# Kernel optimization log

Hardware: AMD Instinct MI355X
Metric: run time of the kernel (lower is better)

The kernel has to match this reference:

```python
import jax, jax.numpy as jnp
import numpy as np

EMB = 1024
HEADS = 16
B, N = 2, 2048

def setup_inputs() -> dict:
    key = jax.random.key(0)
    ks = jax.random.split(key, 9)
    s = 1.0 / np.sqrt(EMB)
    return {
        "x": jax.random.normal(ks[0], (B, N, EMB), dtype=jnp.float32),
        "Wq": jax.random.normal(ks[1], (EMB, EMB), dtype=jnp.float32) * s,
        "bq": jax.random.normal(ks[2], (EMB,), dtype=jnp.float32) * 0.01,
        "Wk": jax.random.normal(ks[3], (EMB, EMB), dtype=jnp.float32) * s,
        "bk": jax.random.normal(ks[4], (EMB,), dtype=jnp.float32) * 0.01,
        "Wv": jax.random.normal(ks[5], (EMB, EMB), dtype=jnp.float32) * s,
        "bv": jax.random.normal(ks[6], (EMB,), dtype=jnp.float32) * 0.01,
        "Wo": jax.random.normal(ks[7], (EMB, EMB), dtype=jnp.float32) * s,
        "bo": jax.random.normal(ks[8], (EMB,), dtype=jnp.float32) * 0.01,
    }

def _split_heads(t):
    b, n, e = t.shape
    return t.reshape(b, n, HEADS, e // HEADS).transpose(0, 2, 1, 3)  # b h n d

def reference(x, Wq, bq, Wk, bk, Wv, bv, Wo, bo):
    q = _split_heads(x @ Wq + bq)
    k = _split_heads(x @ Wk + bk)
    v = _split_heads(x @ Wv + bv)
    # NOTE: original scales by sqrt(emb_size), not sqrt(head_dim)
    scaling = jnp.asarray(EMB, x.dtype) ** 0.5
    energy = jnp.einsum('bhqd,bhkd->bhqk', q, k)
    att = jax.nn.softmax(energy / scaling, axis=-1)
    out = jnp.einsum('bhqk,bhkd->bhqd', att, v)
    out = out.transpose(0, 2, 1, 3).reshape(x.shape[0], x.shape[1], EMB)
    return out @ Wo + bo
```

## Files before the change

### kernel.cpp

```cpp
#include <hip/hip_runtime.h>
#include <hip/hip_bf16.h>

typedef __bf16 bf16_t;
typedef bf16_t bf16x4 __attribute__((ext_vector_type(4)));
typedef bf16_t bf16x8 __attribute__((ext_vector_type(8)));
typedef float f32x4 __attribute__((ext_vector_type(4)));

#define EMB 1024
#define HEADS 16
#define BATCH 2
#define SEQ 2048
#define HD 64
#define TOKENS (BATCH * SEQ)

__device__ __forceinline__ void gld16(bf16_t* lds_dst, const bf16_t* g_src) {
    __builtin_amdgcn_global_load_lds(
        (const __attribute__((address_space(1))) unsigned int*)g_src,
        (__attribute__((address_space(3))) unsigned int*)lds_dst, 16, 0, 0);
}

__global__ __launch_bounds__(256) void convert_x(const float* __restrict__ x,
                                                 bf16_t* __restrict__ xb) {
    size_t i = ((size_t)blockIdx.x * 256 + threadIdx.x) * 16;
    f32x4 v0 = *(const f32x4*)&x[i];
    f32x4 v1 = *(const f32x4*)&x[i + 4];
    f32x4 v2 = *(const f32x4*)&x[i + 8];
    f32x4 v3 = *(const f32x4*)&x[i + 12];
    bf16x8 o0, o1;
#pragma unroll
    for (int j = 0; j < 4; ++j) {
        o0[j] = (bf16_t)v0[j]; o0[4 + j] = (bf16_t)v1[j];
        o1[j] = (bf16_t)v2[j]; o1[4 + j] = (bf16_t)v3[j];
    }
    *(bf16x8*)&xb[i] = o0;
    *(bf16x8*)&xb[i + 8] = o1;
}

__global__ __launch_bounds__(256) void prep_w(
    const float* __restrict__ W0, const float* __restrict__ W1,
    const float* __restrict__ W2, const float* __restrict__ W3,
    bf16_t* __restrict__ T0, bf16_t* __restrict__ T1,
    bf16_t* __restrict__ T2, bf16_t* __restrict__ T3) {
    __shared__ __align__(16) bf16_t T[64][72];
    int z = blockIdx.z;
    const float* src = (z == 0) ? W0 : (z == 1) ? W1 : (z == 2) ? W2 : W3;
    bf16_t* dst = (z == 0) ? T0 : (z == 1) ? T1 : (z == 2) ? T2 : T3;
    int k0 = blockIdx.y * 64, n0 = blockIdx.x * 64;
    int r = threadIdx.x >> 2, c4 = (threadIdx.x & 3) * 16;
    f32x4 v[4];
#pragma unroll
    for (int q = 0; q < 4; ++q)
        v[q] = *(const f32x4*)&src[(size_t)(k0 + r) * 1024 + n0 + c4 + q * 4];
#pragma unroll
    for (int j = 0; j < 16; ++j) T[c4 + j][r] = (bf16_t)v[j >> 2][j & 3];
    __syncthreads();
    bf16x8 o0 = *(const bf16x8*)&T[r][c4];
    bf16x8 o1 = *(const bf16x8*)&T[r][c4 + 8];
    *(bf16x8*)&dst[(size_t)(n0 + r) * 1024 + k0 + c4] = o0;
    *(bf16x8*)&dst[(size_t)(n0 + r) * 1024 + k0 + c4 + 8] = o1;
}

template <typename TO>
__global__ __launch_bounds__(256) void gemm128(
    const bf16_t* __restrict__ A,
    const bf16_t* __restrict__ Wt0, const bf16_t* __restrict__ Wt1, const bf16_t* __restrict__ Wt2,
    const float* __restrict__ b0, const float* __restrict__ b1, const float* __restrict__ b2,
    TO* __restrict__ o0, TO* __restrict__ o1, TO* __restrict__ o2,
    int md0, int md1, int md2, float sc0, float sc1, float sc2) {
    __shared__ __align__(16) bf16_t As[128 * 64];
    __shared__ __align__(16) bf16_t Bs[128 * 64];

    const int tid = threadIdx.x, w = tid >> 6, lane = tid & 63;
    const int quad = lane >> 4, c = lane & 15;
    const int wm = (w >> 1) * 64, wn = (w & 1) * 64;
    const int m0 = blockIdx.y * 128, n0 = blockIdx.x * 128;

    const int z = blockIdx.z;
    const bf16_t* W = (z == 0) ? Wt0 : (z == 1) ? Wt1 : Wt2;
    const float* bias = (z == 0) ? b0 : (z == 1) ? b1 : b2;
    TO* out = (z == 0) ? o0 : (z == 1) ? o1 : o2;
    const int mode = (z == 0) ? md0 : (z == 1) ? md1 : md2;
    const float scale = (z == 0) ? sc0 : (z == 1) ? sc1 : sc2;

    f32x4 acc[4][4];
#pragma unroll
    for (int i = 0; i < 4; ++i)
#pragma unroll
        for (int j = 0; j < 4; ++j) acc[i][j] = (f32x4){0.f, 0.f, 0.f, 0.f};

    const int srow = lane >> 3, sch = lane & 7;
    const int scol = (sch ^ srow) * 8;
    const bf16_t* Ag = A + (size_t)m0 * 1024;
    const bf16_t* Bg = W + (size_t)n0 * 1024;

    for (int k0 = 0; k0 < 1024; k0 += 64) {
        __syncthreads();
#pragma unroll
        for (int s = 0; s < 4; ++s) {
            int rg = (w * 4 + s) * 8;
            gld16(&As[rg * 64], &Ag[(size_t)(rg + srow) * 1024 + k0 + scol]);
            gld16(&Bs[rg * 64], &Bg[(size_t)(rg + srow) * 1024 + k0 + scol]);
        }
        __syncthreads();

#pragma unroll
        for (int ks = 0; ks < 2; ++ks) {
            bf16x8 af[4], bfv[4];
#pragma unroll
            for (int t = 0; t < 4; ++t)
                af[t] = *(const bf16x8*)&As[(wm + t * 16 + c) * 64 +
                                            (((ks * 4 + quad) ^ (c & 7)) * 8)];
#pragma unroll
            for (int t = 0; t < 4; ++t)
                bfv[t] = *(const bf16x8*)&Bs[(wn + t * 16 + c) * 64 +
                                             (((ks * 4 + quad) ^ (c & 7)) * 8)];
#pragma unroll
            for (int mt = 0; mt < 4; ++mt)
#pragma unroll
                for (int nt = 0; nt < 4; ++nt)
                    acc[mt][nt] = __builtin_amdgcn_mfma_f32_16x16x32_bf16(
                        af[mt], bfv[nt], acc[mt][nt], 0, 0, 0);
        }
    }

#pragma unroll
    for (int nt = 0; nt < 4; ++nt) {
        int col = n0 + wn + nt * 16 + c;
        float bv = bias[col];
#pragma unroll
        for (int mt = 0; mt < 4; ++mt)
#pragma unroll
            for (int r = 0; r < 4; ++r) {
                int row = m0 + wm + mt * 16 + quad * 4 + r;
                float v = (acc[mt][nt][r] + bv) * scale;
                size_t idx;
                if (mode == 0) {
                    idx = (size_t)row * 1024 + col;
                } else {
                    int bb = row >> 11, n = row & 2047;
                    int hh = col >> 6, d = col & 63;
                    idx = (mode == 1) ? ((size_t)(bb * HEADS + hh) * SEQ + n) * HD + d
                                      : ((size_t)(bb * HEADS + hh) * HD + d) * SEQ + n;
                }
                out[idx] = (TO)v;
            }
    }
}

__global__ __launch_bounds__(256) void attn_kernel(
    const bf16_t* __restrict__ Q, const bf16_t* __restrict__ K,
    const bf16_t* __restrict__ Vt, bf16_t* __restrict__ O) {
    __shared__ __align__(16) bf16_t Ks[128 * 64];
    __shared__ __align__(16) bf16_t Vs[64 * 128];
    __shared__ __align__(16) bf16_t Ps[4][2][16][72];
    __shared__ float Lbuf[2][2][64];

    const int tid = threadIdx.x, w = tid >> 6, lane = tid & 63;
    const int quad = lane >> 4, c = lane & 15;
    const int qh = w & 1, kh = w >> 1;
    const int bh = blockIdx.x, b = bh >> 4, h = bh & 15;
    const int q0 = blockIdx.y * 64;

    const bf16_t* Qg = Q + ((size_t)bh * SEQ + q0) * HD;
    bf16x8 qf[2][2];
#pragma unroll
    for (int u = 0; u < 2; ++u)
#pragma unroll
        for (int ks = 0; ks < 2; ++ks)
            qf[u][ks] = *(const bf16x8*)&Qg[(qh * 32 + u * 16 + c) * 64 + ks * 32 + quad * 8];

    f32x4 Oacc[2][4];
#pragma unroll
    for (int u = 0; u < 2; ++u)
#pragma unroll
        for (int t = 0; t < 4; ++t) Oacc[u][t] = (f32x4){0.f, 0.f, 0.f, 0.f};
    float lp[2] = {0.f, 0.f};

    const int kr = lane >> 3, kch = lane & 7;
    const int vr = lane >> 4, vch = lane & 15;

    for (int j0 = 0; j0 < SEQ; j0 += 128) {
        __syncthreads();
        const bf16_t* Kg = K + ((size_t)bh * SEQ + j0) * HD;
        const bf16_t* Vg = Vt + (size_t)bh * HD * SEQ + j0;
#pragma unroll
        for (int s = 0; s < 4; ++s) {
            int krg = w * 32 + s * 8, krow = krg + kr;
            gld16(&Ks[krg * 64], &Kg[(size_t)krow * 64 + (kch ^ (krow & 7)) * 8]);
            int vrg = w * 16 + s * 4, vrow = vrg + vr;
            gld16(&Vs[vrg * 128], &Vg[(size_t)vrow * SEQ + (vch ^ (vrow & 15)) * 8]);
        }
        __syncthreads();

        f32x4 S[2][4];
#pragma unroll
        for (int u = 0; u < 2; ++u)
#pragma unroll
            for (int t = 0; t < 4; ++t) S[u][t] = (f32x4){0.f, 0.f, 0.f, 0.f};
#pragma unroll
        for (int ks = 0; ks < 2; ++ks)
#pragma unroll
            for (int t = 0; t < 4; ++t) {
                int row = kh * 64 + t * 16 + c;
                bf16x8 kv = *(const bf16x8*)&Ks[row * 64 + (((ks * 4 + quad) ^ (c & 7)) * 8)];
                S[0][t] = __builtin_amdgcn_mfma_f32_16x16x32_bf16(kv, qf[0][ks], S[0][t], 0, 0, 0);
                S[1][t] = __builtin_amdgcn_mfma_f32_16x16x32_bf16(kv, qf[1][ks], S[1][t], 0, 0, 0);
            }

#pragma unroll
        for (int u = 0; u < 2; ++u)
#pragma unroll
            for (int t = 0; t < 4; ++t) {
                bf16x4 pk;
#pragma unroll
                for (int r = 0; r < 4; ++r) {
                    float p = __builtin_amdgcn_exp2f(S[u][t][r]);
                    lp[u] += p;
                    pk[r] = (bf16_t)p;
                }
                *(bf16x4*)&Ps[w][u][c][t * 16 + quad * 4] = pk;
            }

#pragma unroll
        for (int ks2 = 0; ks2 < 2; ++ks2) {
            bf16x8 af0 = *(const bf16x8*)&Ps[w][0][c][ks2 * 32 + quad * 8];
            bf16x8 af1 = *(const bf16x8*)&Ps[w][1][c][ks2 * 32 + quad * 8];
#pragma unroll
            for (int t = 0; t < 4; ++t) {
                int row = t * 16 + c;
                bf16x8 vv = *(const bf16x8*)&Vs[row * 128 + (((kh * 8 + ks2 * 4 + quad) ^ c) * 8)];
                Oacc[0][t] = __builtin_amdgcn_mfma_f32_16x16x32_bf16(af0, vv, Oacc[0][t], 0, 0, 0);
                Oacc[1][t] = __builtin_amdgcn_mfma_f32_16x16x32_bf16(af1, vv, Oacc[1][t], 0, 0, 0);
            }
        }
    }

#pragma unroll
    for (int u = 0; u < 2; ++u) {
        lp[u] += __shfl_xor(lp[u], 16);
        lp[u] += __shfl_xor(lp[u], 32);
    }

    __syncthreads();
    float* Obuf = (float*)Ks;
    if (kh == 1) {
#pragma unroll
        for (int u = 0; u < 2; ++u) {
#pragma unroll
            for (int t = 0; t < 4; ++t)
                *(f32x4*)&Obuf[(((qh * 2 + u) * 4 + t) * 64 + lane) * 4] = Oacc[u][t];
            Lbuf[qh][u][lane] = lp[u];
        }
    }
    __syncthreads();
    if (kh == 0) {
        float lr[2][4];
#pragma unroll
        for (int u = 0; u < 2; ++u) {
            lp[u] += Lbuf[qh][u][lane];
#pragma unroll
            for (int r = 0; r < 4; ++r) lr[u][r] = __shfl(lp[u], quad * 4 + r);
        }
#pragma unroll
        for (int u = 0; u < 2; ++u)
#pragma unroll
            for (int t = 0; t < 4; ++t) {
                f32x4 part = *(const f32x4*)&Obuf[(((qh * 2 + u) * 4 + t) * 64 + lane) * 4];
#pragma unroll
                for (int r = 0; r < 4; ++r) {
                    int qrow = q0 + qh * 32 + u * 16 + quad * 4 + r;
                    size_t idx = ((size_t)(b * SEQ + qrow)) * EMB + h * 64 + t * 16 + c;
                    O[idx] = (bf16_t)((Oacc[u][t][r] + part[r]) / lr[u][r]);
                }
            }
    }
}

extern "C" void kernel_launch(void* const* d_in, const int* in_sizes, int n_in,
                              void* d_out, int out_size, void* d_ws, size_t ws_size,
                              hipStream_t stream) {
    (void)in_sizes; (void)n_in; (void)out_size; (void)ws_size;
    const float* x  = (const float*)d_in[0];
    const float* Wq = (const float*)d_in[1];
    const float* bq = (const float*)d_in[2];
    const float* Wk = (const float*)d_in[3];
    const float* bk = (const float*)d_in[4];
    const float* Wv = (const float*)d_in[5];
    const float* bv = (const float*)d_in[6];
    const float* Wo = (const float*)d_in[7];
    const float* bo = (const float*)d_in[8];

    bf16_t* ws = (bf16_t*)d_ws;
    const size_t NELEM = (size_t)TOKENS * EMB;
    const size_t WELEM = (size_t)EMB * EMB;
    bf16_t* Qb  = ws;
    bf16_t* Kb  = ws + NELEM;
    bf16_t* Vtb = ws + 2 * NELEM;
    bf16_t* Ob  = ws + 3 * NELEM;
    bf16_t* xb  = ws + 4 * NELEM;
    bf16_t* Wt0 = ws + 5 * NELEM;
    bf16_t* Wt1 = Wt0 + WELEM;
    bf16_t* Wt2 = Wt0 + 2 * WELEM;
    bf16_t* Wt3 = Wt0 + 3 * WELEM;

    const float QSCALE = 1.4426950408889634f / 32.0f;

    hipLaunchKernelGGL(convert_x, dim3(1024), dim3(256), 0, stream, x, xb);
    hipLaunchKernelGGL(prep_w, dim3(16, 16, 4), dim3(256), 0, stream,
                       Wq, Wk, Wv, Wo, Wt0, Wt1, Wt2, Wt3);
    hipLaunchKernelGGL((gemm128<bf16_t>), dim3(8, 32, 3), dim3(256), 0, stream,
                       xb, Wt0, Wt1, Wt2, bq, bk, bv, Qb, Kb, Vtb,
                       1, 1, 2, QSCALE, 1.0f, 1.0f);
    hipLaunchKernelGGL(attn_kernel, dim3(32, 32), dim3(256), 0, stream, Qb, Kb, Vtb, Ob);
    hipLaunchKernelGGL((gemm128<float>), dim3(8, 32, 1), dim3(256), 0, stream,
                       Ob, Wt3, Wt3, Wt3, bo, bo, bo,
                       (float*)d_out, (float*)d_out, (float*)d_out,
                       0, 0, 0, 1.0f, 1.0f, 1.0f);
}
```

Measured before the change: 233.6 us.

## Shrink GEMM tiles to 64x128 and register-prefetch K/V tiles in attention

The projection GEMMs switch from 128x128 tiles with K-step 64 to 64x128 tiles with K-step 32 and no LDS swizzle. This doubles the grid to raise occupancy and CU coverage, at the cost of more syncs per K and more LDS bank conflicts. The attention kernel replaces direct global-to-LDS loads with register prefetch of the next K/V tile, stored to LDS after the barrier, so global latency overlaps compute. The swizzle now moves from the LDS address to the global read address, which costs registers and adds an extra VGPR-to-LDS store step.

```diff
diff --git a/kernel.cpp b/kernel.cpp
--- a/kernel.cpp
+++ b/kernel.cpp
@@ -61,19 +61,19 @@
 }
 
 template <typename TO>
-__global__ __launch_bounds__(256) void gemm128(
+__global__ __launch_bounds__(256) void gemm64(
     const bf16_t* __restrict__ A,
     const bf16_t* __restrict__ Wt0, const bf16_t* __restrict__ Wt1, const bf16_t* __restrict__ Wt2,
     const float* __restrict__ b0, const float* __restrict__ b1, const float* __restrict__ b2,
     TO* __restrict__ o0, TO* __restrict__ o1, TO* __restrict__ o2,
     int md0, int md1, int md2, float sc0, float sc1, float sc2) {
-    __shared__ __align__(16) bf16_t As[128 * 64];
-    __shared__ __align__(16) bf16_t Bs[128 * 64];
+    __shared__ __align__(16) bf16_t As[64 * 32];
+    __shared__ __align__(16) bf16_t Bs[128 * 32];
 
     const int tid = threadIdx.x, w = tid >> 6, lane = tid & 63;
     const int quad = lane >> 4, c = lane & 15;
-    const int wm = (w >> 1) * 64, wn = (w & 1) * 64;
-    const int m0 = blockIdx.y * 128, n0 = blockIdx.x * 128;
+    const int wm = (w >> 1) * 32, wn = (w & 1) * 64;
+    const int m0 = blockIdx.y * 64, n0 = blockIdx.x * 128;
 
     const int z = blockIdx.z;
     const bf16_t* W = (z == 0) ? Wt0 : (z == 1) ? Wt1 : Wt2;
@@ -82,45 +82,39 @@
     const int mode = (z == 0) ? md0 : (z == 1) ? md1 : md2;
     const float scale = (z == 0) ? sc0 : (z == 1) ? sc1 : sc2;
 
-    f32x4 acc[4][4];
-#pragma unroll
-    for (int i = 0; i < 4; ++i)
+    f32x4 acc[2][4];
+#pragma unroll
+    for (int i = 0; i < 2; ++i)
 #pragma unroll
         for (int j = 0; j < 4; ++j) acc[i][j] = (f32x4){0.f, 0.f, 0.f, 0.f};
 
-    const int srow = lane >> 3, sch = lane & 7;
-    const int scol = (sch ^ srow) * 8;
+    const int srow = lane >> 2, sch = lane & 3;
     const bf16_t* Ag = A + (size_t)m0 * 1024;
     const bf16_t* Bg = W + (size_t)n0 * 1024;
 
-    for (int k0 = 0; k0 < 1024; k0 += 64) {
+    for (int k0 = 0; k0 < 1024; k0 += 32) {
         __syncthreads();
-#pragma unroll
-        for (int s = 0; s < 4; ++s) {
-            int rg = (w * 4 + s) * 8;
-            gld16(&As[rg * 64], &Ag[(size_t)(rg + srow) * 1024 + k0 + scol]);
-            gld16(&Bs[rg * 64], &Bg[(size_t)(rg + srow) * 1024 + k0 + scol]);
+        gld16(&As[(w * 16) * 32], &Ag[(size_t)(w * 16 + srow) * 1024 + k0 + sch * 8]);
+#pragma unroll
+        for (int s = 0; s < 2; ++s) {
+            int rg = w * 32 + s * 16;
+            gld16(&Bs[rg * 32], &Bg[(size_t)(rg + srow) * 1024 + k0 + sch * 8]);
         }
         __syncthreads();
 
-#pragma unroll
-        for (int ks = 0; ks < 2; ++ks) {
-            bf16x8 af[4], bfv[4];
-#pragma unroll
-            for (int t = 0; t < 4; ++t)
-                af[t] = *(const bf16x8*)&As[(wm + t * 16 + c) * 64 +
-                                            (((ks * 4 + quad) ^ (c & 7)) * 8)];
-#pragma unroll
-            for (int t = 0; t < 4; ++t)
-                bfv[t] = *(const bf16x8*)&Bs[(wn + t * 16 + c) * 64 +
-                                             (((ks * 4 + quad) ^ (c & 7)) * 8)];
-#pragma unroll
-            for (int mt = 0; mt < 4; ++mt)
-#pragma unroll
-                for (int nt = 0; nt < 4; ++nt)
-                    acc[mt][nt] = __builtin_amdgcn_mfma_f32_16x16x32_bf16(
-                        af[mt], bfv[nt], acc[mt][nt], 0, 0, 0);
-        }
+        bf16x8 af[2], bfv[4];
+#pragma unroll
+        for (int t = 0; t < 2; ++t)
+            af[t] = *(const bf16x8*)&As[(wm + t * 16 + c) * 32 + quad * 8];
+#pragma unroll
+        for (int t = 0; t < 4; ++t)
+            bfv[t] = *(const bf16x8*)&Bs[(wn + t * 16 + c) * 32 + quad * 8];
+#pragma unroll
+        for (int mt = 0; mt < 2; ++mt)
+#pragma unroll
+            for (int nt = 0; nt < 4; ++nt)
+                acc[mt][nt] = __builtin_amdgcn_mfma_f32_16x16x32_bf16(
+                    af[mt], bfv[nt], acc[mt][nt], 0, 0, 0);
     }
 
 #pragma unroll
@@ -128,7 +122,7 @@
         int col = n0 + wn + nt * 16 + c;
         float bv = bias[col];
 #pragma unroll
-        for (int mt = 0; mt < 4; ++mt)
+        for (int mt = 0; mt < 2; ++mt)
 #pragma unroll
             for (int r = 0; r < 4; ++r) {
                 int row = m0 + wm + mt * 16 + quad * 4 + r;
@@ -179,18 +173,32 @@
     const int kr = lane >> 3, kch = lane & 7;
     const int vr = lane >> 4, vch = lane & 15;
 
+    const bf16_t* Kg = K + (size_t)bh * SEQ * HD;
+    const bf16_t* Vg = Vt + (size_t)bh * HD * SEQ;
+
+    bf16x8 kbuf[4], vbuf[4];
+    auto load_tile = [&](int j0) {
+#pragma unroll
+        for (int s = 0; s < 4; ++s) {
+            int krow = w * 32 + s * 8 + kr;
+            kbuf[s] = *(const bf16x8*)&Kg[(size_t)(j0 + krow) * 64 + (kch ^ kr) * 8];
+            int vrow = w * 16 + s * 4 + vr;
+            vbuf[s] = *(const bf16x8*)&Vg[(size_t)vrow * SEQ + j0 + (vch ^ (vrow & 15)) * 8];
+        }
+    };
+    load_tile(0);
+
     for (int j0 = 0; j0 < SEQ; j0 += 128) {
         __syncthreads();
-        const bf16_t* Kg = K + ((size_t)bh * SEQ + j0) * HD;
-        const bf16_t* Vg = Vt + (size_t)bh * HD * SEQ + j0;
 #pragma unroll
         for (int s = 0; s < 4; ++s) {
-            int krg = w * 32 + s * 8, krow = krg + kr;
-            gld16(&Ks[krg * 64], &Kg[(size_t)krow * 64 + (kch ^ (krow & 7)) * 8]);
-            int vrg = w * 16 + s * 4, vrow = vrg + vr;
-            gld16(&Vs[vrg * 128], &Vg[(size_t)vrow * SEQ + (vch ^ (vrow & 15)) * 8]);
+            int krow = w * 32 + s * 8 + kr;
+            *(bf16x8*)&Ks[krow * 64 + kch * 8] = kbuf[s];
+            int vrow = w * 16 + s * 4 + vr;
+            *(bf16x8*)&Vs[vrow * 128 + vch * 8] = vbuf[s];
         }
         __syncthreads();
+        if (j0 + 128 < SEQ) load_tile(j0 + 128);
 
         f32x4 S[2][4];
 #pragma unroll
@@ -308,11 +316,11 @@
     hipLaunchKernelGGL(convert_x, dim3(1024), dim3(256), 0, stream, x, xb);
     hipLaunchKernelGGL(prep_w, dim3(16, 16, 4), dim3(256), 0, stream,
                        Wq, Wk, Wv, Wo, Wt0, Wt1, Wt2, Wt3);
-    hipLaunchKernelGGL((gemm128<bf16_t>), dim3(8, 32, 3), dim3(256), 0, stream,
+    hipLaunchKernelGGL((gemm64<bf16_t>), dim3(8, 64, 3), dim3(256), 0, stream,
                        xb, Wt0, Wt1, Wt2, bq, bk, bv, Qb, Kb, Vtb,
                        1, 1, 2, QSCALE, 1.0f, 1.0f);
     hipLaunchKernelGGL(attn_kernel, dim3(32, 32), dim3(256), 0, stream, Qb, Kb, Vtb, Ob);
-    hipLaunchKernelGGL((gemm128<float>), dim3(8, 32, 1), dim3(256), 0, stream,
+    hipLaunchKernelGGL((gemm64<float>), dim3(8, 64, 1), dim3(256), 0, stream,
                        Ob, Wt3, Wt3, Wt3, bo, bo, bo,
                        (float*)d_out, (float*)d_out, (float*)d_out,
                        0, 0, 0, 1.0f, 1.0f, 1.0f);
```

Result: no change. 231.7 us (-0.8%).
